# Performance work log

Measured on AMD Instinct MI355X. Metric: run time of the kernel, lower is better.

The kernel has to match this reference:

```python
import jax, jax.numpy as jnp
import numpy as np

N_NODES = 50000
N_EDGES = 1600000


def gcn_conv(h, W, b, src, dst, ew, n_nodes):
    """PyG GCNConv: linear -> add self-loops (weight 1) -> sym-norm scatter-add -> bias."""
    h = h @ W                                   # [N, out]
    loop = jnp.arange(n_nodes, dtype=src.dtype)
    s = jnp.concatenate([src, loop])            # [E+N]
    d = jnp.concatenate([dst, loop])
    w = jnp.concatenate([ew, jnp.ones((n_nodes,), dtype=h.dtype)])
    deg = jax.ops.segment_sum(w, d, num_segments=n_nodes)          # in-degree (weighted)
    dinv = jnp.where(deg > 0, jax.lax.rsqrt(deg), 0.0)
    coef = dinv[s] * w * dinv[d]                # D^-1/2 A D^-1/2 per-edge coefficient
    msg = h[s] * coef[:, None]                  # gather + scale  [E+N, out]
    out = jax.ops.segment_sum(msg, d, num_segments=n_nodes)        # scatter-add
    return out + b


def setup_inputs() -> dict:
    key = jax.random.key(0)
    ks = jax.random.split(key, 6)
    x = jax.random.normal(ks[0], (N_NODES, 256), dtype=jnp.float32)
    edge_index = jax.random.randint(ks[1], (2, N_EDGES), 0, N_NODES, dtype=jnp.int64)
    edge_weight = jax.random.uniform(ks[2], (N_EDGES,), dtype=jnp.float32)
    W1 = jax.random.normal(ks[3], (256, 128), dtype=jnp.float32) * (1.0 / np.sqrt(256))
    b1 = jnp.zeros((128,), dtype=jnp.float32)
    W2 = jax.random.normal(ks[4], (128, 64), dtype=jnp.float32) * (1.0 / np.sqrt(128))
    b2 = jnp.zeros((64,), dtype=jnp.float32)
    return {"x": x, "edge_index": edge_index, "edge_weight": edge_weight,
            "W1": W1, "b1": b1, "W2": W2, "b2": b2}


def reference(x, edge_index, edge_weight, W1, b1, W2, b2):
    src, dst = edge_index[0], edge_index[1]
    n = x.shape[0]
    h = gcn_conv(x, W1, b1, src, dst, edge_weight, n)
    h = jax.nn.relu(h)
    # dropout is identity in eval mode
    out = gcn_conv(h, W2, b2, src, dst, edge_weight, n)
    return out
```

## Files before the change

### kernel.cpp

```cpp
#include <hip/hip_runtime.h>

#define NN 50000
#define NE 1600000
#define NB 391
#define NBLK 128
#define NSEG 50048

typedef short bf16x8 __attribute__((ext_vector_type(8)));
typedef float f32x4 __attribute__((ext_vector_type(4)));

static __device__ __forceinline__ unsigned f2bf(float f) {
    union { float f; unsigned u; } v; v.f = f;
    return (v.u + 0x7FFF + ((v.u >> 16) & 1)) >> 16;
}

__global__ __launch_bounds__(256) void p1_hist(const int* __restrict__ dst,
        int* __restrict__ cntB) {
    __shared__ int h[NB];
    for (int i = threadIdx.x; i < NB; i += 256) h[i] = 0;
    __syncthreads();
    int base = blockIdx.x * 12500;
    for (int k = threadIdx.x; k < 12500; k += 256)
        atomicAdd(&h[dst[base + k] >> 7], 1);
    __syncthreads();
    for (int i = threadIdx.x; i < NB; i += 256)
        cntB[i * NBLK + blockIdx.x] = h[i];
}

__global__ __launch_bounds__(256) void scan1_kernel(const int* __restrict__ in,
        int* __restrict__ csum, int* __restrict__ bsum) {
    __shared__ int sd[256];
    int t = threadIdx.x;
    int idx = blockIdx.x * 256 + t;
    int v = (idx < NSEG) ? in[idx] : 0;
    sd[t] = v;
    __syncthreads();
    for (int off = 1; off < 256; off <<= 1) {
        int x = (t >= off) ? sd[t - off] : 0;
        __syncthreads();
        sd[t] += x;
        __syncthreads();
    }
    if (idx < NSEG) csum[idx + 1] = sd[t];
    if (t == 255) bsum[blockIdx.x] = sd[255];
}

__global__ __launch_bounds__(256) void scan2_kernel(int* __restrict__ bsum,
        int* __restrict__ csum) {
    __shared__ int sd[256];
    int t = threadIdx.x;
    int v = (t < 196) ? bsum[t] : 0;
    sd[t] = v;
    __syncthreads();
    for (int off = 1; off < 256; off <<= 1) {
        int x = (t >= off) ? sd[t - off] : 0;
        __syncthreads();
        sd[t] += x;
        __syncthreads();
    }
    if (t < 196) bsum[t] = sd[t] - v;
    if (t == 0) csum[0] = 0;
}

__global__ __launch_bounds__(256) void scan3_kernel(int* __restrict__ csum,
        const int* __restrict__ bsum) {
    int idx = blockIdx.x * 256 + threadIdx.x;
    if (idx < NSEG) csum[idx + 1] += bsum[blockIdx.x];
}

__global__ __launch_bounds__(256) void p3_scatter(const int* __restrict__ src,
        const int* __restrict__ dst, const float* __restrict__ ew,
        const int* __restrict__ csum, int2* __restrict__ ebuf) {
    __shared__ int curs[NB];
    for (int i = threadIdx.x; i < NB; i += 256)
        curs[i] = csum[i * NBLK + blockIdx.x];
    __syncthreads();
    int base = blockIdx.x * 12500;
    for (int k = threadIdx.x; k < 12500; k += 256) {
        int d = dst[base + k];
        int s = src[base + k];
        float w = ew[base + k];
        int pos = atomicAdd(&curs[d >> 7], 1);
        ebuf[pos] = make_int2(s | ((d & 127) << 16), __float_as_int(w));
    }
}

__global__ __launch_bounds__(256) void p4_build(const int2* __restrict__ ebuf,
        const int* __restrict__ csum, int2* __restrict__ edata,
        float* __restrict__ dinv, int* __restrict__ rowptr) {
    __shared__ int cnt[128], loff[128], cur[128], sd[128];
    __shared__ float deg[128];
    int bk = blockIdx.x;
    int t = threadIdx.x;
    int ebase = csum[bk * 128];
    int ecnt = csum[(bk + 1) * 128] - ebase;
    if (t < 128) { cnt[t] = 0; cur[t] = 0; deg[t] = 0.0f; }
    __syncthreads();
    for (int i = t; i < ecnt; i += 256) {
        int2 e = ebuf[ebase + i];
        int dl = (e.x >> 16) & 127;
        atomicAdd(&cnt[dl], 1);
        atomicAdd(&deg[dl], __int_as_float(e.y));
    }
    __syncthreads();
    if (t < 128) sd[t] = cnt[t];
    __syncthreads();
    for (int off = 1; off < 128; off <<= 1) {
        int v = 0;
        if (t < 128 && t >= off) v = sd[t - off];
        __syncthreads();
        if (t < 128) sd[t] += v;
        __syncthreads();
    }
    if (t < 128) loff[t] = sd[t] - cnt[t];
    __syncthreads();
    int node = bk * 128 + t;
    if (t < 128 && node < NN) {
        dinv[node] = rsqrtf(deg[t] + 1.0f);
        rowptr[node] = ebase + loff[t];
    }
    if (bk == NB - 1 && t == 0) rowptr[NN] = NE;
    for (int i = t; i < ecnt; i += 256) {
        int2 e = ebuf[ebase + i];
        int dl = (e.x >> 16) & 127;
        int slot = loff[dl] + atomicAdd(&cur[dl], 1);
        edata[ebase + slot] = make_int2(e.x & 0xFFFF, e.y);
    }
}

__global__ __launch_bounds__(256) void wt_kernel(const float* __restrict__ W1,
        const float* __restrict__ W2, ushort* __restrict__ Wt1,
        ushort* __restrict__ Wt2) {
    int idx = blockIdx.x * 256 + threadIdx.x;
    if (idx < 32768) {
        int k = idx >> 7, n = idx & 127;
        Wt1[n * 256 + k] = (ushort)f2bf(W1[idx]);
    } else if (idx < 40960) {
        int i = idx - 32768;
        int k = i >> 6, n = i & 63;
        Wt2[n * 128 + k] = (ushort)f2bf(W2[i]);
    }
}

__global__ __launch_bounds__(256) void gemm1_kernel(const float* __restrict__ A,
        const ushort* __restrict__ Bt, ushort* __restrict__ C,
        const float* __restrict__ dinv, int M) {
    const int K = 256, N = 128;
    __shared__ __align__(16) ushort As[64][72];
    __shared__ __align__(16) ushort Bs[128][72];
    int tid = threadIdx.x;
    int bm = blockIdx.x * 64;
    int w = tid >> 6, lane = tid & 63;
    int m = lane & 15, quad = lane >> 4;
    f32x4 acc[8] = {};
    int ra = tid >> 2, ksa = (tid & 3) * 16;
    int rb = tid >> 1, ksb = (tid & 1) * 32;
    int grow = bm + ra; if (grow >= M) grow = M - 1;
    const float* ap = A + (size_t)grow * K + ksa;
    const ushort* bp = Bt + (size_t)rb * K + ksb;
    for (int k0 = 0; k0 < K; k0 += 64) {
        float4 f0 = *(const float4*)(ap + k0);
        float4 f1 = *(const float4*)(ap + k0 + 4);
        float4 f2 = *(const float4*)(ap + k0 + 8);
        float4 f3 = *(const float4*)(ap + k0 + 12);
        uint4 bv0 = *(const uint4*)(bp + k0);
        uint4 bv1 = *(const uint4*)(bp + k0 + 8);
        uint4 bv2 = *(const uint4*)(bp + k0 + 16);
        uint4 bv3 = *(const uint4*)(bp + k0 + 24);
        uint4 pa, pb;
        pa.x = f2bf(f0.x) | (f2bf(f0.y) << 16);
        pa.y = f2bf(f0.z) | (f2bf(f0.w) << 16);
        pa.z = f2bf(f1.x) | (f2bf(f1.y) << 16);
        pa.w = f2bf(f1.z) | (f2bf(f1.w) << 16);
        pb.x = f2bf(f2.x) | (f2bf(f2.y) << 16);
        pb.y = f2bf(f2.z) | (f2bf(f2.w) << 16);
        pb.z = f2bf(f3.x) | (f2bf(f3.y) << 16);
        pb.w = f2bf(f3.z) | (f2bf(f3.w) << 16);
        __syncthreads();
        *(uint4*)&As[ra][ksa] = pa;
        *(uint4*)&As[ra][ksa + 8] = pb;
        *(uint4*)&Bs[rb][ksb] = bv0;
        *(uint4*)&Bs[rb][ksb + 8] = bv1;
        *(uint4*)&Bs[rb][ksb + 16] = bv2;
        *(uint4*)&Bs[rb][ksb + 24] = bv3;
        __syncthreads();
        #pragma unroll
        for (int ks = 0; ks < 2; ++ks) {
            bf16x8 a = *(const bf16x8*)&As[w * 16 + m][ks * 32 + quad * 8];
            #pragma unroll
            for (int t = 0; t < 8; ++t) {
                bf16x8 b = *(const bf16x8*)&Bs[t * 16 + m][ks * 32 + quad * 8];
                acc[t] = __builtin_amdgcn_mfma_f32_16x16x32_bf16(a, b, acc[t], 0, 0, 0);
            }
        }
    }
    int rbase = bm + w * 16 + quad * 4;
    float dv[4];
    #pragma unroll
    for (int rg = 0; rg < 4; ++rg)
        dv[rg] = (rbase + rg < M) ? dinv[rbase + rg] : 0.0f;
    #pragma unroll
    for (int t = 0; t < 8; ++t) {
        int col = t * 16 + m;
        #pragma unroll
        for (int rg = 0; rg < 4; ++rg) {
            int row = rbase + rg;
            if (row < M)
                C[(size_t)row * N + col] = (ushort)f2bf(dv[rg] * acc[t][rg]);
        }
    }
}

__global__ __launch_bounds__(256) void agg1_fused_kernel(
        const int* __restrict__ rowptr, const int2* __restrict__ edata,
        const ushort* __restrict__ H, const float* __restrict__ dinv,
        const float* __restrict__ bias, const ushort* __restrict__ Wt2,
        ushort* __restrict__ H2) {
    __shared__ __align__(16) ushort Ats[16][136];
    int tid = threadIdx.x;
    int nl = tid >> 4;
    int node = blockIdx.x * 16 + nl;
    int glane = tid & 15;
    int gb = (tid & 63) & ~15;
    int beg = rowptr[node], end = rowptr[node + 1];
    float acc[8] = {};
    const ushort* Hl = H + (size_t)glane * 8;
    for (int chunk = beg; chunk < end; chunk += 16) {
        int nch = end - chunk; if (nch > 16) nch = 16;
        int edx = 0, edy = 0;
        if (glane < nch) {
            int2 e = edata[chunk + glane];
            edx = e.x; edy = e.y;
        }
        int j = 0;
        for (; j + 2 <= nch; j += 2) {
            int s0 = __shfl(edx, gb + j);
            int s1 = __shfl(edx, gb + j + 1);
            float c0 = __int_as_float(__shfl(edy, gb + j));
            float c1 = __int_as_float(__shfl(edy, gb + j + 1));
            uint4 h0 = *(const uint4*)(Hl + (size_t)s0 * 128);
            uint4 h1 = *(const uint4*)(Hl + (size_t)s1 * 128);
            const unsigned* u0 = (const unsigned*)&h0;
            const unsigned* u1 = (const unsigned*)&h1;
            #pragma unroll
            for (int q = 0; q < 4; ++q) {
                acc[2*q]   += __uint_as_float(u0[q] << 16) * c0;
                acc[2*q+1] += __uint_as_float(u0[q] & 0xFFFF0000u) * c0;
            }
            #pragma unroll
            for (int q = 0; q < 4; ++q) {
                acc[2*q]   += __uint_as_float(u1[q] << 16) * c1;
                acc[2*q+1] += __uint_as_float(u1[q] & 0xFFFF0000u) * c1;
            }
        }
        if (j < nch) {
            int s0 = __shfl(edx, gb + j);
            float c0 = __int_as_float(__shfl(edy, gb + j));
            uint4 h0 = *(const uint4*)(Hl + (size_t)s0 * 128);
            const unsigned* u0 = (const unsigned*)&h0;
            #pragma unroll
            for (int q = 0; q < 4; ++q) {
                acc[2*q]   += __uint_as_float(u0[q] << 16) * c0;
                acc[2*q+1] += __uint_as_float(u0[q] & 0xFFFF0000u) * c0;
            }
        }
    }
    float di = dinv[node];
    uint4 hn = *(const uint4*)(Hl + (size_t)node * 128);
    const unsigned* un = (const unsigned*)&hn;
    float4 bv0 = *(const float4*)(bias + glane * 8);
    float4 bv1 = *(const float4*)(bias + glane * 8 + 4);
    float v[8];
    #pragma unroll
    for (int q = 0; q < 4; ++q) {
        v[2*q]   = di * (acc[2*q]   + __uint_as_float(un[q] << 16));
        v[2*q+1] = di * (acc[2*q+1] + __uint_as_float(un[q] & 0xFFFF0000u));
    }
    v[0] += bv0.x; v[1] += bv0.y; v[2] += bv0.z; v[3] += bv0.w;
    v[4] += bv1.x; v[5] += bv1.y; v[6] += bv1.z; v[7] += bv1.w;
    #pragma unroll
    for (int k = 0; k < 8; ++k) v[k] = fmaxf(v[k], 0.0f);
    uint4 o;
    o.x = f2bf(v[0]) | (f2bf(v[1]) << 16);
    o.y = f2bf(v[2]) | (f2bf(v[3]) << 16);
    o.z = f2bf(v[4]) | (f2bf(v[5]) << 16);
    o.w = f2bf(v[6]) | (f2bf(v[7]) << 16);
    *(uint4*)&Ats[nl][glane * 8] = o;
    __syncthreads();
    int w = tid >> 6, lane = tid & 63;
    int m = lane & 15, quad = lane >> 4;
    const ushort* bp = Wt2 + (size_t)(w * 16 + m) * 128 + quad * 8;
    f32x4 c2 = {};
    #pragma unroll
    for (int kc = 0; kc < 4; ++kc) {
        bf16x8 a = *(const bf16x8*)&Ats[m][kc * 32 + quad * 8];
        bf16x8 b = *(const bf16x8*)(bp + kc * 32);
        c2 = __builtin_amdgcn_mfma_f32_16x16x32_bf16(a, b, c2, 0, 0, 0);
    }
    int rbase = blockIdx.x * 16 + quad * 4;
    #pragma unroll
    for (int rg = 0; rg < 4; ++rg) {
        float dvr = dinv[rbase + rg];
        H2[(size_t)(rbase + rg) * 64 + w * 16 + m] = (ushort)f2bf(dvr * c2[rg]);
    }
}

template<int F, int LPN, int RELU, int OUTBF>
__global__ __launch_bounds__(256) void agg_csr_kernel(
        const int* __restrict__ rowptr, const int2* __restrict__ edata,
        const ushort* __restrict__ H, const float* __restrict__ dinv,
        const float* __restrict__ bias, void* __restrict__ outv) {
    constexpr int NPB = 256 / LPN;
    int node = blockIdx.x * NPB + threadIdx.x / LPN;
    if (node >= NN) return;
    int glane = threadIdx.x & (LPN - 1);
    int gb = (threadIdx.x & 63) & ~(LPN - 1);
    int beg = rowptr[node], end = rowptr[node + 1];
    float acc[8] = {};
    const ushort* Hl = H + (size_t)glane * 8;
    for (int chunk = beg; chunk < end; chunk += LPN) {
        int nch = end - chunk; if (nch > LPN) nch = LPN;
        int edx = 0, edy = 0;
        if (glane < nch) {
            int2 e = edata[chunk + glane];
            edx = e.x; edy = e.y;
        }
        int j = 0;
        for (; j + 2 <= nch; j += 2) {
            int s0 = __shfl(edx, gb + j);
            int s1 = __shfl(edx, gb + j + 1);
            float c0 = __int_as_float(__shfl(edy, gb + j));
            float c1 = __int_as_float(__shfl(edy, gb + j + 1));
            uint4 h0 = *(const uint4*)(Hl + (size_t)s0 * F);
            uint4 h1 = *(const uint4*)(Hl + (size_t)s1 * F);
            const unsigned* u0 = (const unsigned*)&h0;
            const unsigned* u1 = (const unsigned*)&h1;
            #pragma unroll
            for (int q = 0; q < 4; ++q) {
                acc[2*q]   += __uint_as_float(u0[q] << 16) * c0;
                acc[2*q+1] += __uint_as_float(u0[q] & 0xFFFF0000u) * c0;
            }
            #pragma unroll
            for (int q = 0; q < 4; ++q) {
                acc[2*q]   += __uint_as_float(u1[q] << 16) * c1;
                acc[2*q+1] += __uint_as_float(u1[q] & 0xFFFF0000u) * c1;
            }
        }
        if (j < nch) {
            int s0 = __shfl(edx, gb + j);
            float c0 = __int_as_float(__shfl(edy, gb + j));
            uint4 h0 = *(const uint4*)(Hl + (size_t)s0 * F);
            const unsigned* u0 = (const unsigned*)&h0;
            #pragma unroll
            for (int q = 0; q < 4; ++q) {
                acc[2*q]   += __uint_as_float(u0[q] << 16) * c0;
                acc[2*q+1] += __uint_as_float(u0[q] & 0xFFFF0000u) * c0;
            }
        }
    }
    float di = dinv[node];
    uint4 hn = *(const uint4*)(Hl + (size_t)node * F);
    const unsigned* un = (const unsigned*)&hn;
    float4 bv0 = *(const float4*)(bias + glane * 8);
    float4 bv1 = *(const float4*)(bias + glane * 8 + 4);
    float v[8];
    #pragma unroll
    for (int q = 0; q < 4; ++q) {
        v[2*q]   = di * (acc[2*q]   + __uint_as_float(un[q] << 16));
        v[2*q+1] = di * (acc[2*q+1] + __uint_as_float(un[q] & 0xFFFF0000u));
    }
    v[0] += bv0.x; v[1] += bv0.y; v[2] += bv0.z; v[3] += bv0.w;
    v[4] += bv1.x; v[5] += bv1.y; v[6] += bv1.z; v[7] += bv1.w;
    if (RELU) {
        #pragma unroll
        for (int k = 0; k < 8; ++k) v[k] = fmaxf(v[k], 0.0f);
    }
    if (OUTBF) {
        uint4 o;
        o.x = f2bf(v[0]) | (f2bf(v[1]) << 16);
        o.y = f2bf(v[2]) | (f2bf(v[3]) << 16);
        o.z = f2bf(v[4]) | (f2bf(v[5]) << 16);
        o.w = f2bf(v[6]) | (f2bf(v[7]) << 16);
        *(uint4*)((ushort*)outv + (size_t)node * F + glane * 8) = o;
    } else {
        float* o = (float*)outv + (size_t)node * F + glane * 8;
        *(float4*)(o)     = make_float4(v[0], v[1], v[2], v[3]);
        *(float4*)(o + 4) = make_float4(v[4], v[5], v[6], v[7]);
    }
}

extern "C" void kernel_launch(void* const* d_in, const int* in_sizes, int n_in,
                              void* d_out, int out_size, void* d_ws, size_t ws_size,
                              hipStream_t stream) {
    const float* x  = (const float*)d_in[0];
    const int*   ei = (const int*)d_in[1];
    const float* ew = (const float*)d_in[2];
    const float* W1 = (const float*)d_in[3];
    const float* b1 = (const float*)d_in[4];
    const float* W2 = (const float*)d_in[5];
    const float* b2 = (const float*)d_in[6];
    const int* src = ei;
    const int* dst = ei + NE;
    float* out = (float*)d_out;

    float* ws     = (float*)d_ws;
    float* dinv   = ws;
    int*   rowptr = (int*)(ws + 50048);
    int*   csum   = (int*)(ws + 100112);
    int*   bsum   = (int*)(ws + 150176);
    int*   cntB   = (int*)(ws + 150528);
    ushort* Wt1   = (ushort*)(ws + 200576);
    ushort* Wt2   = Wt1 + 32768;
    int2*  edata  = (int2*)(ws + 221056);
    ushort* H1    = (ushort*)(ws + 3421056);
    ushort* H2    = (ushort*)(ws + 6621056);
    int2*  ebuf   = (int2*)H2;

    p1_hist<<<NBLK, 256, 0, stream>>>(dst, cntB);
    scan1_kernel<<<196, 256, 0, stream>>>(cntB, csum, bsum);
    scan2_kernel<<<1, 256, 0, stream>>>(bsum, csum);
    scan3_kernel<<<196, 256, 0, stream>>>(csum, bsum);
    wt_kernel<<<160, 256, 0, stream>>>(W1, W2, Wt1, Wt2);
    p3_scatter<<<NBLK, 256, 0, stream>>>(src, dst, ew, csum, ebuf);
    p4_build<<<NB, 256, 0, stream>>>(ebuf, csum, edata, dinv, rowptr);

    gemm1_kernel<<<782, 256, 0, stream>>>(x, Wt1, H1, dinv, NN);
    agg1_fused_kernel<<<3125, 256, 0, stream>>>(rowptr, edata, H1, dinv, b1, Wt2, H2);
    agg_csr_kernel<64, 8, 0, 0><<<1563, 256, 0, stream>>>(rowptr, edata, H2, dinv, b2, out);
}
```

Baseline: 266.4 us.

## Merge CSR build phases into one cooperative kernel with grid syncs

Replaces seven small preprocessing kernels (histogram, three-stage scan, weight transpose, scatter, per-bucket build) with a single cooperative launch of 391 blocks that separates the phases with grid.sync(). The weight transpose now runs on the blocks left idle during the histogram phase. This removes several kernel launch gaps and tail effects, but adds grid-wide barrier costs and requires all 391 blocks to be co-resident, which holds easily on this GPU.

```diff
diff --git a/kernel.cpp b/kernel.cpp
--- a/kernel.cpp
+++ b/kernel.cpp
@@ -1,4 +1,7 @@
 #include <hip/hip_runtime.h>
+#include <hip/hip_cooperative_groups.h>
+
+namespace cg = cooperative_groups;
 
 #define NN 50000
 #define NE 1600000
@@ -14,131 +17,139 @@
     return (v.u + 0x7FFF + ((v.u >> 16) & 1)) >> 16;
 }
 
-__global__ __launch_bounds__(256) void p1_hist(const int* __restrict__ dst,
-        int* __restrict__ cntB) {
-    __shared__ int h[NB];
-    for (int i = threadIdx.x; i < NB; i += 256) h[i] = 0;
-    __syncthreads();
-    int base = blockIdx.x * 12500;
-    for (int k = threadIdx.x; k < 12500; k += 256)
-        atomicAdd(&h[dst[base + k] >> 7], 1);
-    __syncthreads();
-    for (int i = threadIdx.x; i < NB; i += 256)
-        cntB[i * NBLK + blockIdx.x] = h[i];
-}
-
-__global__ __launch_bounds__(256) void scan1_kernel(const int* __restrict__ in,
-        int* __restrict__ csum, int* __restrict__ bsum) {
-    __shared__ int sd[256];
+__global__ __launch_bounds__(256) void build_kernel(
+        const int* __restrict__ src, const int* __restrict__ dst,
+        const float* __restrict__ ew, const float* __restrict__ W1,
+        const float* __restrict__ W2, int* __restrict__ cntB,
+        int* __restrict__ csum, int* __restrict__ bsum,
+        ushort* __restrict__ Wt1, ushort* __restrict__ Wt2,
+        int2* __restrict__ ebuf, int2* __restrict__ edata,
+        float* __restrict__ dinv, int* __restrict__ rowptr) {
+    cg::grid_group grid = cg::this_grid();
+    __shared__ int smem[640];
     int t = threadIdx.x;
-    int idx = blockIdx.x * 256 + t;
-    int v = (idx < NSEG) ? in[idx] : 0;
-    sd[t] = v;
-    __syncthreads();
-    for (int off = 1; off < 256; off <<= 1) {
-        int x = (t >= off) ? sd[t - off] : 0;
-        __syncthreads();
-        sd[t] += x;
-        __syncthreads();
-    }
-    if (idx < NSEG) csum[idx + 1] = sd[t];
-    if (t == 255) bsum[blockIdx.x] = sd[255];
-}
-
-__global__ __launch_bounds__(256) void scan2_kernel(int* __restrict__ bsum,
-        int* __restrict__ csum) {
-    __shared__ int sd[256];
-    int t = threadIdx.x;
-    int v = (t < 196) ? bsum[t] : 0;
-    sd[t] = v;
-    __syncthreads();
-    for (int off = 1; off < 256; off <<= 1) {
-        int x = (t >= off) ? sd[t - off] : 0;
-        __syncthreads();
-        sd[t] += x;
-        __syncthreads();
-    }
-    if (t < 196) bsum[t] = sd[t] - v;
-    if (t == 0) csum[0] = 0;
-}
-
-__global__ __launch_bounds__(256) void scan3_kernel(int* __restrict__ csum,
-        const int* __restrict__ bsum) {
-    int idx = blockIdx.x * 256 + threadIdx.x;
-    if (idx < NSEG) csum[idx + 1] += bsum[blockIdx.x];
-}
-
-__global__ __launch_bounds__(256) void p3_scatter(const int* __restrict__ src,
-        const int* __restrict__ dst, const float* __restrict__ ew,
-        const int* __restrict__ csum, int2* __restrict__ ebuf) {
-    __shared__ int curs[NB];
-    for (int i = threadIdx.x; i < NB; i += 256)
-        curs[i] = csum[i * NBLK + blockIdx.x];
-    __syncthreads();
-    int base = blockIdx.x * 12500;
-    for (int k = threadIdx.x; k < 12500; k += 256) {
-        int d = dst[base + k];
-        int s = src[base + k];
-        float w = ew[base + k];
-        int pos = atomicAdd(&curs[d >> 7], 1);
-        ebuf[pos] = make_int2(s | ((d & 127) << 16), __float_as_int(w));
-    }
-}
-
-__global__ __launch_bounds__(256) void p4_build(const int2* __restrict__ ebuf,
-        const int* __restrict__ csum, int2* __restrict__ edata,
-        float* __restrict__ dinv, int* __restrict__ rowptr) {
-    __shared__ int cnt[128], loff[128], cur[128], sd[128];
-    __shared__ float deg[128];
-    int bk = blockIdx.x;
-    int t = threadIdx.x;
-    int ebase = csum[bk * 128];
-    int ecnt = csum[(bk + 1) * 128] - ebase;
-    if (t < 128) { cnt[t] = 0; cur[t] = 0; deg[t] = 0.0f; }
-    __syncthreads();
-    for (int i = t; i < ecnt; i += 256) {
-        int2 e = ebuf[ebase + i];
-        int dl = (e.x >> 16) & 127;
-        atomicAdd(&cnt[dl], 1);
-        atomicAdd(&deg[dl], __int_as_float(e.y));
-    }
-    __syncthreads();
-    if (t < 128) sd[t] = cnt[t];
-    __syncthreads();
-    for (int off = 1; off < 128; off <<= 1) {
-        int v = 0;
-        if (t < 128 && t >= off) v = sd[t - off];
-        __syncthreads();
-        if (t < 128) sd[t] += v;
-        __syncthreads();
-    }
-    if (t < 128) loff[t] = sd[t] - cnt[t];
-    __syncthreads();
-    int node = bk * 128 + t;
-    if (t < 128 && node < NN) {
-        dinv[node] = rsqrtf(deg[t] + 1.0f);
-        rowptr[node] = ebase + loff[t];
-    }
-    if (bk == NB - 1 && t == 0) rowptr[NN] = NE;
-    for (int i = t; i < ecnt; i += 256) {
-        int2 e = ebuf[ebase + i];
-        int dl = (e.x >> 16) & 127;
-        int slot = loff[dl] + atomicAdd(&cur[dl], 1);
-        edata[ebase + slot] = make_int2(e.x & 0xFFFF, e.y);
-    }
-}
-
-__global__ __launch_bounds__(256) void wt_kernel(const float* __restrict__ W1,
-        const float* __restrict__ W2, ushort* __restrict__ Wt1,
-        ushort* __restrict__ Wt2) {
-    int idx = blockIdx.x * 256 + threadIdx.x;
-    if (idx < 32768) {
-        int k = idx >> 7, n = idx & 127;
-        Wt1[n * 256 + k] = (ushort)f2bf(W1[idx]);
-    } else if (idx < 40960) {
-        int i = idx - 32768;
-        int k = i >> 6, n = i & 63;
-        Wt2[n * 128 + k] = (ushort)f2bf(W2[i]);
+    int blk = blockIdx.x;
+
+    if (blk < NBLK) {
+        int* h = smem;
+        for (int i = t; i < NB; i += 256) h[i] = 0;
+        __syncthreads();
+        int base = blk * 12500;
+        for (int k = t; k < 12500; k += 256)
+            atomicAdd(&h[dst[base + k] >> 7], 1);
+        __syncthreads();
+        for (int i = t; i < NB; i += 256)
+            cntB[i * NBLK + blk] = h[i];
+    } else {
+        for (int idx = (blk - NBLK) * 256 + t; idx < 40960; idx += (NB - NBLK) * 256) {
+            if (idx < 32768) {
+                int k = idx >> 7, n = idx & 127;
+                Wt1[n * 256 + k] = (ushort)f2bf(W1[idx]);
+            } else {
+                int i = idx - 32768;
+                int k = i >> 6, n = i & 63;
+                Wt2[n * 128 + k] = (ushort)f2bf(W2[i]);
+            }
+        }
+    }
+    grid.sync();
+
+    if (blk < 196) {
+        int* sd = smem;
+        int idx = blk * 256 + t;
+        int v = (idx < NSEG) ? cntB[idx] : 0;
+        sd[t] = v;
+        __syncthreads();
+        for (int off = 1; off < 256; off <<= 1) {
+            int x = (t >= off) ? sd[t - off] : 0;
+            __syncthreads();
+            sd[t] += x;
+            __syncthreads();
+        }
+        if (idx < NSEG) csum[idx + 1] = sd[t];
+        if (t == 255) bsum[blk] = sd[255];
+    }
+    grid.sync();
+
+    if (blk == 0) {
+        int* sd = smem;
+        int v = (t < 196) ? bsum[t] : 0;
+        sd[t] = v;
+        __syncthreads();
+        for (int off = 1; off < 256; off <<= 1) {
+            int x = (t >= off) ? sd[t - off] : 0;
+            __syncthreads();
+            sd[t] += x;
+            __syncthreads();
+        }
+        if (t < 196) bsum[t] = sd[t] - v;
+        if (t == 0) csum[0] = 0;
+    }
+    grid.sync();
+
+    if (blk < 196) {
+        int idx = blk * 256 + t;
+        if (idx < NSEG) csum[idx + 1] += bsum[blk];
+    }
+    grid.sync();
+
+    if (blk < NBLK) {
+        int* curs = smem;
+        for (int i = t; i < NB; i += 256)
+            curs[i] = csum[i * NBLK + blk];
+        __syncthreads();
+        int base = blk * 12500;
+        for (int k = t; k < 12500; k += 256) {
+            int d = dst[base + k];
+            int s = src[base + k];
+            float w = ew[base + k];
+            int pos = atomicAdd(&curs[d >> 7], 1);
+            ebuf[pos] = make_int2(s | ((d & 127) << 16), __float_as_int(w));
+        }
+    }
+    grid.sync();
+
+    {
+        int* cnt  = smem;
+        int* loff = smem + 128;
+        int* cur  = smem + 256;
+        int* sd   = smem + 384;
+        float* deg = (float*)(smem + 512);
+        int bk = blk;
+        int ebase = csum[bk * 128];
+        int ecnt = csum[(bk + 1) * 128] - ebase;
+        if (t < 128) { cnt[t] = 0; cur[t] = 0; deg[t] = 0.0f; }
+        __syncthreads();
+        for (int i = t; i < ecnt; i += 256) {
+            int2 e = ebuf[ebase + i];
+            int dl = (e.x >> 16) & 127;
+            atomicAdd(&cnt[dl], 1);
+            atomicAdd(&deg[dl], __int_as_float(e.y));
+        }
+        __syncthreads();
+        if (t < 128) sd[t] = cnt[t];
+        __syncthreads();
+        for (int off = 1; off < 128; off <<= 1) {
+            int v = 0;
+            if (t < 128 && t >= off) v = sd[t - off];
+            __syncthreads();
+            if (t < 128) sd[t] += v;
+            __syncthreads();
+        }
+        if (t < 128) loff[t] = sd[t] - cnt[t];
+        __syncthreads();
+        int node = bk * 128 + t;
+        if (t < 128 && node < NN) {
+            dinv[node] = rsqrtf(deg[t] + 1.0f);
+            rowptr[node] = ebase + loff[t];
+        }
+        if (bk == NB - 1 && t == 0) rowptr[NN] = NE;
+        for (int i = t; i < ecnt; i += 256) {
+            int2 e = ebuf[ebase + i];
+            int dl = (e.x >> 16) & 127;
+            int slot = loff[dl] + atomicAdd(&cur[dl], 1);
+            edata[ebase + slot] = make_int2(e.x & 0xFFFF, e.y);
+        }
     }
 }
 
@@ -416,13 +427,10 @@
     ushort* H2    = (ushort*)(ws + 6621056);
     int2*  ebuf   = (int2*)H2;
 
-    p1_hist<<<NBLK, 256, 0, stream>>>(dst, cntB);
-    scan1_kernel<<<196, 256, 0, stream>>>(cntB, csum, bsum);
-    scan2_kernel<<<1, 256, 0, stream>>>(bsum, csum);
-    scan3_kernel<<<196, 256, 0, stream>>>(csum, bsum);
-    wt_kernel<<<160, 256, 0, stream>>>(W1, W2, Wt1, Wt2);
-    p3_scatter<<<NBLK, 256, 0, stream>>>(src, dst, ew, csum, ebuf);
-    p4_build<<<NB, 256, 0, stream>>>(ebuf, csum, edata, dinv, rowptr);
+    void* kargs[] = {(void*)&src, (void*)&dst, (void*)&ew, (void*)&W1, (void*)&W2,
+                     (void*)&cntB, (void*)&csum, (void*)&bsum, (void*)&Wt1, (void*)&Wt2,
+                     (void*)&ebuf, (void*)&edata, (void*)&dinv, (void*)&rowptr};
+    hipLaunchCooperativeKernel((void*)build_kernel, dim3(NB), dim3(256), kargs, 0, stream);
 
     gemm1_kernel<<<782, 256, 0, stream>>>(x, Wt1, H1, dinv, NN);
     agg1_fused_kernel<<<3125, 256, 0, stream>>>(rowptr, edata, H1, dinv, b1, Wt2, H2);
```

After: 492.4 us. 1.85x slower.
